# Performance work log

Measured on AMD Instinct MI355X. Metric: run time of the kernel, lower is better.

## Reference

```python
import jax, jax.numpy as jnp
import numpy as np

MEAN = 0.0
SIGMA = 2.0


def setup_inputs() -> dict:
    key = jax.random.key(0)
    B, S, D = 8, 1024, 1024
    ks = jax.random.split(key, 7)
    scale = 1.0 / np.sqrt(D)
    return {
        "x": jax.random.normal(ks[0], (B, S, D), dtype=jnp.float32),
        "Wa": jax.random.normal(ks[1], (D, D), dtype=jnp.float32) * scale,
        "ba": jnp.zeros((D,), dtype=jnp.float32),
        "Wshift": jax.random.normal(ks[2], (D, D), dtype=jnp.float32) * scale,
        "bshift": jnp.zeros((D,), dtype=jnp.float32),
        "Wscale": jax.random.normal(ks[3], (D, D), dtype=jnp.float32) * scale,
        "bscale": jnp.zeros((D,), dtype=jnp.float32),
    }


def _gaussian_matrix(S, dtype):
    # Row t holds the flipped, normalized Gaussian kernel of length t+1:
    # weight on position j (j<=t) is exp(-((t-j)-mean)^2/(2*sigma^2)), row-normalized.
    idx = jnp.arange(S)
    d = idx[:, None] - idx[None, :]  # t - j
    g = jnp.exp(-((d.astype(dtype) - MEAN) ** 2) / (2.0 * SIGMA ** 2))
    g = jnp.where(d >= 0, g, 0.0)  # causal (growing window)
    return g / jnp.sum(g, axis=1, keepdims=True)


def reference(x, Wa, ba, Wshift, bshift, Wscale, bscale):
    S = x.shape[1]
    W = _gaussian_matrix(S, x.dtype)  # [S, S] lower-triangular
    filtered = jnp.einsum("tj,bjd->btd", W, x)  # causal Gaussian-weighted sum
    shift = filtered @ Wshift + bshift
    scale = filtered @ Wscale + bscale
    affine = jax.nn.relu(x @ Wa + ba)
    return scale * affine + shift
```

## Files before the change

kernel.cpp:

```cpp
#include <hip/hip_runtime.h>
#include <stdint.h>

typedef __attribute__((ext_vector_type(8))) __bf16 bf16x8;
typedef __attribute__((ext_vector_type(4))) float f32x4;

__device__ __forceinline__ unsigned short f2bf(float f) {
  union { float f; unsigned int u; } v; v.f = f;
  unsigned int u = v.u;
  u = (u + 0x7FFFu + ((u >> 16) & 1u)) >> 16;
  return (unsigned short)u;
}
__device__ __forceinline__ float bf2f(unsigned int u) {
  union { unsigned int u; float f; } v; v.u = u << 16;
  return v.f;
}

__global__ __launch_bounds__(256) void prep(
    const float* __restrict__ x, unsigned short* __restrict__ xb,
    const float* __restrict__ Wa, const float* __restrict__ Wsh,
    const float* __restrict__ Wsc, unsigned short* __restrict__ Wt3)
{
  __shared__ float t[64][65];
  int bid = blockIdx.x;
  if (bid < 4096) {
    const size_t i = ((size_t)bid * 256 + threadIdx.x) * 8;
    const float4 a = *(const float4*)(x + i);
    const float4 b = *(const float4*)(x + i + 4);
    ushort4 o0, o1;
    o0.x = f2bf(a.x); o0.y = f2bf(a.y); o0.z = f2bf(a.z); o0.w = f2bf(a.w);
    o1.x = f2bf(b.x); o1.y = f2bf(b.y); o1.z = f2bf(b.z); o1.w = f2bf(b.w);
    *(ushort4*)(xb + i) = o0;
    *(ushort4*)(xb + i + 4) = o1;
    return;
  }
  bid -= 4096;
  const int z  = bid >> 8;
  const int yy = (bid >> 4) & 15;
  const int xx = bid & 15;
  const float* W = (z == 0) ? Wa : (z == 1) ? Wsh : Wsc;
  unsigned short* O = Wt3 + ((size_t)z << 20);
  const int k0 = xx * 64;
  const int n0 = yy * 64;
  const int r = threadIdx.x >> 4;
  const int c4 = threadIdx.x & 15;
#pragma unroll
  for (int i = 0; i < 4; ++i) {
    const int row = r + i * 16;
    const float4 v = *(const float4*)(W + (size_t)(k0 + row) * 1024 + n0 + c4 * 4);
    t[row][c4 * 4 + 0] = v.x; t[row][c4 * 4 + 1] = v.y;
    t[row][c4 * 4 + 2] = v.z; t[row][c4 * 4 + 3] = v.w;
  }
  __syncthreads();
#pragma unroll
  for (int i = 0; i < 4; ++i) {
    const int nr = r + i * 16;
    ushort4 o;
    o.x = f2bf(t[c4 * 4 + 0][nr]);
    o.y = f2bf(t[c4 * 4 + 1][nr]);
    o.z = f2bf(t[c4 * 4 + 2][nr]);
    o.w = f2bf(t[c4 * 4 + 3][nr]);
    *(ushort4*)(O + (size_t)(n0 + nr) * 1024 + k0 + c4 * 4) = o;
  }
}

__global__ __launch_bounds__(512, 2) void gemm_all(
    const unsigned short* __restrict__ xb, const unsigned short* __restrict__ Wt3,
    const float* __restrict__ ba, const float* __restrict__ bsh,
    const float* __restrict__ bsc, float* __restrict__ out)
{
  __shared__ __attribute__((aligned(16))) char lds[118784];
  unsigned short* const sX0 = (unsigned short*)lds;
  unsigned short* const sX1 = (unsigned short*)(lds + 34816);
  unsigned short* const sB0 = (unsigned short*)(lds + 69632);
  unsigned short* const sB1 = (unsigned short*)(lds + 94208);
  unsigned short* const ysh_l = (unsigned short*)lds;
  unsigned short* const ysc_l = (unsigned short*)(lds + 35072);
  unsigned short* const aff_l = (unsigned short*)(lds + 70144);

  const int tid = threadIdx.x;
  const int lane = tid & 63;
  const int wid = tid >> 6;
  const int wm = wid >> 1;
  const int wn = wid & 1;
  const int lr = lane & 15;
  const int lk = lane >> 4;

  const int bid = blockIdx.x;
  const int xcd = bid & 7;
  const int rr_ = bid >> 3;
  const int ntl = rr_ & 15;
  const int mg  = rr_ >> 4;
  const int bm0 = (xcd + (mg << 3)) * 256;
  const int bn0 = ntl * 64;
  const bool first = ((bm0 & 1023) == 0);

  f32x4 acc[3][4][2];
  f32x4 hacc[2][2];
  const f32x4 z = {0.f, 0.f, 0.f, 0.f};
#pragma unroll
  for (int a = 0; a < 3; ++a)
#pragma unroll
    for (int m = 0; m < 4; ++m)
#pragma unroll
      for (int j = 0; j < 2; ++j) acc[a][m][j] = z;
#pragma unroll
  for (int a = 0; a < 2; ++a)
#pragma unroll
    for (int j = 0; j < 2; ++j) hacc[a][j] = z;

  auto stage = [&](int k0, unsigned short* dX, unsigned short* dB) {
#pragma unroll
    for (int p = 0; p < 4; ++p) {
      const int po = (p * 512 + tid) * 16;
      const int row = po >> 7;
      const int lo = po ^ ((row & 7) << 4);
      const int colu = (lo & 127) >> 1;
      const unsigned short* src = xb + (size_t)(bm0 + row) * 1024 + k0 + colu;
      __builtin_amdgcn_global_load_lds(
          (const __attribute__((address_space(1))) void*)src,
          (__attribute__((address_space(3))) void*)(dX + (p * 512 + (wid << 6)) * 8),
          16, 0, 0);
    }
    if (tid < 128) {
      const int po = (2048 + tid) * 16;
      const int row = po >> 7;
      const int lo = po ^ ((row & 7) << 4);
      const int colu = (lo & 127) >> 1;
      int grow = bm0 - 16 + (row - 256);
      if (first) grow = bm0;
      const unsigned short* src = xb + (size_t)grow * 1024 + k0 + colu;
      __builtin_amdgcn_global_load_lds(
          (const __attribute__((address_space(1))) void*)src,
          (__attribute__((address_space(3))) void*)(dX + (2048 + (wid << 6)) * 8),
          16, 0, 0);
    }
#pragma unroll
    for (int mat = 0; mat < 3; ++mat) {
      const int po = tid * 16;
      const int row = po >> 7;
      const int lo = po ^ ((row & 7) << 4);
      const int colu = (lo & 127) >> 1;
      const unsigned short* src =
          Wt3 + ((size_t)mat << 20) + (size_t)(bn0 + row) * 1024 + k0 + colu;
      __builtin_amdgcn_global_load_lds(
          (const __attribute__((address_space(1))) void*)src,
          (__attribute__((address_space(3))) void*)(dB + mat * 4096 + (wid << 6) * 8),
          16, 0, 0);
    }
  };
  auto rd = [&](const unsigned short* base, int row, int s) -> bf16x8 {
    const int po = row * 128 + (((s * 32 + lk * 8) * 2) ^ ((row & 7) << 4));
    return *(const bf16x8*)((const char*)base + po);
  };

  stage(0, sX0, sB0);
  unsigned short *sXc = sX0, *sBc = sB0, *sXn = sX1, *sBn = sB1;

  for (int kt = 0; kt < 16; ++kt) {
    if (kt + 1 < 16) stage((kt + 1) * 64, sXn, sBn);

    if (kt + 1 < 16) {
      if (wid < 2) asm volatile("s_waitcnt vmcnt(8)" ::: "memory");
      else         asm volatile("s_waitcnt vmcnt(7)" ::: "memory");
    } else {
      asm volatile("s_waitcnt vmcnt(0)" ::: "memory");
    }
    __builtin_amdgcn_s_barrier();
    asm volatile("" ::: "memory");

#pragma unroll
    for (int s = 0; s < 2; ++s) {
      bf16x8 ax[4], bb[3][2], hax;
#pragma unroll
      for (int m = 0; m < 4; ++m)
        ax[m] = rd(sXc, wm * 64 + m * 16 + lr, s);
#pragma unroll
      for (int mat = 0; mat < 3; ++mat)
#pragma unroll
        for (int jj = 0; jj < 2; ++jj)
          bb[mat][jj] = rd(sBc + mat * 4096, wn * 32 + jj * 16 + lr, s);
      if (wm == 0) hax = rd(sXc, 256 + lr, s);

      __builtin_amdgcn_s_setprio(1);
#pragma unroll
      for (int m = 0; m < 4; ++m)
#pragma unroll
        for (int mat = 0; mat < 3; ++mat)
#pragma unroll
          for (int jj = 0; jj < 2; ++jj)
            acc[mat][m][jj] = __builtin_amdgcn_mfma_f32_16x16x32_bf16(
                ax[m], bb[mat][jj], acc[mat][m][jj], 0, 0, 0);
      if (wm == 0) {
#pragma unroll
        for (int mat = 1; mat < 3; ++mat)
#pragma unroll
          for (int jj = 0; jj < 2; ++jj)
            hacc[mat - 1][jj] = __builtin_amdgcn_mfma_f32_16x16x32_bf16(
                hax, bb[mat][jj], hacc[mat - 1][jj], 0, 0, 0);
      }
      __builtin_amdgcn_s_setprio(0);
    }

    asm volatile("s_waitcnt lgkmcnt(0)" ::: "memory");
    __builtin_amdgcn_s_barrier();
    asm volatile("" ::: "memory");

    unsigned short* t1 = sXc; sXc = sXn; sXn = t1;
    unsigned short* t2 = sBc; sBc = sBn; sBn = t2;
  }

#pragma unroll
  for (int jj = 0; jj < 2; ++jj) {
    const int nn = wn * 32 + jj * 16 + lr;
    const float Ba = ba[bn0 + nn];
#pragma unroll
    for (int m = 0; m < 4; ++m)
#pragma unroll
      for (int q = 0; q < 4; ++q) {
        const int rowL = wm * 64 + m * 16 + lk * 4 + q;
        aff_l[nn * 258 + rowL] = f2bf(fmaxf(acc[0][m][jj][q] + Ba, 0.0f));
        ysh_l[nn * 274 + 15 + rowL] = f2bf(acc[1][m][jj][q]);
        ysc_l[nn * 274 + 15 + rowL] = f2bf(acc[2][m][jj][q]);
      }
    if (wm == 0) {
#pragma unroll
      for (int q = 0; q < 4; ++q) {
        const int hr = lk * 4 + q;
        if (hr > 0) {
          ysh_l[nn * 274 + hr - 1] = f2bf(hacc[0][jj][q]);
          ysc_l[nn * 274 + hr - 1] = f2bf(hacc[1][jj][q]);
        }
      }
    }
  }
  __syncthreads();
  if (first) {
    for (int i = tid; i < 64 * 15; i += 512) {
      const int nn = i / 15, rw = i % 15;
      ysh_l[nn * 274 + rw] = 0;
      ysc_l[nn * 274 + rw] = 0;
    }
  }
  __syncthreads();

  {
    const int nn = tid & 63;
    const int t0 = (tid >> 6) * 32;
    float g[16];
#pragma unroll
    for (int k = 0; k < 16; ++k) g[k] = __expf(-(float)(k * k) * 0.125f);
    float nfull = 0.f;
#pragma unroll
    for (int k = 0; k < 16; ++k) nfull += g[k];
    const float invf = 1.0f / nfull;
    const float bs = bsh[bn0 + nn];
    const float bc = bsc[bn0 + nn];

    float psh[15], psc[15];
#pragma unroll
    for (int i = 0; i < 15; ++i) {
      psh[i] = bf2f(ysh_l[nn * 274 + t0 + i]);
      psc[i] = bf2f(ysc_l[nn * 274 + t0 + i]);
    }

    for (int c = 0; c < 2; ++c) {
      const int T = t0 + c * 16;
      float csh[16], csc[16], av[16];
#pragma unroll
      for (int u = 0; u < 16; ++u) {
        csh[u] = bf2f(ysh_l[nn * 274 + 15 + T + u]);
        csc[u] = bf2f(ysc_l[nn * 274 + 15 + T + u]);
        av[u]  = bf2f(aff_l[nn * 258 + T + u]);
      }
#pragma unroll
      for (int u = 0; u < 16; ++u) {
        float fs = 0.f, fc = 0.f;
#pragma unroll
        for (int k = 0; k < 16; ++k) {
          const int d = u - k;
          const float vs = (d >= 0) ? csh[d] : psh[15 + d];
          const float vc = (d >= 0) ? csc[d] : psc[15 + d];
          fs = fmaf(g[k], vs, fs);
          fc = fmaf(g[k], vc, fc);
        }
        float inv = invf;
        if (first && (T + u) < 15) {
          float sum = 0.f;
#pragma unroll
          for (int k = 0; k < 16; ++k) sum += (k <= T + u) ? g[k] : 0.f;
          inv = 1.0f / sum;
        }
        out[(size_t)(bm0 + T + u) * 1024 + bn0 + nn] =
            (fc * inv + bc) * av[u] + (fs * inv + bs);
      }
#pragma unroll
      for (int i = 0; i < 15; ++i) { psh[i] = csh[i + 1]; psc[i] = csc[i + 1]; }
    }
  }
}

extern "C" void kernel_launch(void* const* d_in, const int* in_sizes, int n_in,
                              void* d_out, int out_size, void* d_ws, size_t ws_size,
                              hipStream_t stream) {
  const float* x   = (const float*)d_in[0];
  const float* Wa  = (const float*)d_in[1];
  const float* ba  = (const float*)d_in[2];
  const float* Wsh = (const float*)d_in[3];
  const float* bsh = (const float*)d_in[4];
  const float* Wsc = (const float*)d_in[5];
  const float* bsc = (const float*)d_in[6];
  float* out = (float*)d_out;

  char* ws = (char*)d_ws;
  unsigned short* xb  = (unsigned short*)(ws);
  unsigned short* Wt3 = (unsigned short*)(ws + (16u << 20));

  hipLaunchKernelGGL(prep, dim3(4096 + 768), dim3(256), 0, stream,
                     x, xb, Wa, Wsh, Wsc, Wt3);
  hipLaunchKernelGGL(gemm_all, dim3(512), dim3(512), 0, stream,
                     xb, Wt3, ba, bsh, bsc, out);
}
```

Measured before the change: 79.39 us.

## Switch GEMM mainloop to triple-buffered K=32 stages with precomputed load addresses

The fused three-matrix GEMM loop moves from double-buffered K=64 tiles to a three-slot ring of K=32 tiles, prefetching two stages ahead. Global-to-LDS source addresses and destination offsets are computed once per thread, and the copy work is spread across all waves with a new two-rows-per-128B-line swizzle. The aim is to keep more memory traffic in flight, hide load latency, and shrink the LDS footprint. The cost is twice as many barriers per K step and hand-tuned vmcnt counts that must match the per-wave load counts exactly.

```diff
diff --git a/kernel.cpp b/kernel.cpp
--- a/kernel.cpp
+++ b/kernel.cpp
@@ -68,11 +68,8 @@
     const float* __restrict__ ba, const float* __restrict__ bsh,
     const float* __restrict__ bsc, float* __restrict__ out)
 {
-  __shared__ __attribute__((aligned(16))) char lds[118784];
-  unsigned short* const sX0 = (unsigned short*)lds;
-  unsigned short* const sX1 = (unsigned short*)(lds + 34816);
-  unsigned short* const sB0 = (unsigned short*)(lds + 69632);
-  unsigned short* const sB1 = (unsigned short*)(lds + 94208);
+  __shared__ __attribute__((aligned(16))) char lds[103168];
+  constexpr int SLOT = 29696;
   unsigned short* const ysh_l = (unsigned short*)lds;
   unsigned short* const ysc_l = (unsigned short*)(lds + 35072);
   unsigned short* const aff_l = (unsigned short*)(lds + 70144);
@@ -108,105 +105,104 @@
 #pragma unroll
     for (int j = 0; j < 2; ++j) hacc[a][j] = z;
 
-  auto stage = [&](int k0, unsigned short* dX, unsigned short* dB) {
+  const unsigned short* sbase[4];
+  int doff[4];
+#pragma unroll
+  for (int p = 0; p < 4; ++p) {
+    const int gid = p * 8 + wid;
+    sbase[p] = nullptr; doff[p] = 0;
+    if (gid < 17) {
+      const int po = gid * 1024 + (lane << 4);
+      const int line = po >> 7;
+      const int il = (po & 127) ^ ((line & 7) << 4);
+      const int row = line * 2 + (il >> 6);
+      const int colu = (il & 63) >> 1;
+      int grow = (row < 256) ? (bm0 + row)
+                             : (first ? bm0 : bm0 - 16 + (row - 256));
+      sbase[p] = xb + (size_t)grow * 1024 + colu;
+      doff[p] = gid * 1024;
+    } else if (gid < 29) {
+      const int pb = (gid - 17) * 1024 + (lane << 4);
+      const int line = pb >> 7;
+      const int il = (pb & 127) ^ ((line & 7) << 4);
+      const int mat = line >> 5;
+      const int rowm = ((line & 31) << 1) + (il >> 6);
+      const int colu = (il & 63) >> 1;
+      sbase[p] = Wt3 + ((size_t)mat << 20) + (size_t)(bn0 + rowm) * 1024 + colu;
+      doff[p] = 17408 + (gid - 17) * 1024;
+    }
+  }
+
+  auto stage = [&](int k0, char* slot) {
 #pragma unroll
     for (int p = 0; p < 4; ++p) {
-      const int po = (p * 512 + tid) * 16;
-      const int row = po >> 7;
-      const int lo = po ^ ((row & 7) << 4);
-      const int colu = (lo & 127) >> 1;
-      const unsigned short* src = xb + (size_t)(bm0 + row) * 1024 + k0 + colu;
-      __builtin_amdgcn_global_load_lds(
-          (const __attribute__((address_space(1))) void*)src,
-          (__attribute__((address_space(3))) void*)(dX + (p * 512 + (wid << 6)) * 8),
-          16, 0, 0);
-    }
-    if (tid < 128) {
-      const int po = (2048 + tid) * 16;
-      const int row = po >> 7;
-      const int lo = po ^ ((row & 7) << 4);
-      const int colu = (lo & 127) >> 1;
-      int grow = bm0 - 16 + (row - 256);
-      if (first) grow = bm0;
-      const unsigned short* src = xb + (size_t)grow * 1024 + k0 + colu;
-      __builtin_amdgcn_global_load_lds(
-          (const __attribute__((address_space(1))) void*)src,
-          (__attribute__((address_space(3))) void*)(dX + (2048 + (wid << 6)) * 8),
-          16, 0, 0);
-    }
-#pragma unroll
-    for (int mat = 0; mat < 3; ++mat) {
-      const int po = tid * 16;
-      const int row = po >> 7;
-      const int lo = po ^ ((row & 7) << 4);
-      const int colu = (lo & 127) >> 1;
-      const unsigned short* src =
-          Wt3 + ((size_t)mat << 20) + (size_t)(bn0 + row) * 1024 + k0 + colu;
-      __builtin_amdgcn_global_load_lds(
-          (const __attribute__((address_space(1))) void*)src,
-          (__attribute__((address_space(3))) void*)(dB + mat * 4096 + (wid << 6) * 8),
-          16, 0, 0);
+      if (p * 8 + wid < 29) {
+        __builtin_amdgcn_global_load_lds(
+            (const __attribute__((address_space(1))) void*)(sbase[p] + k0),
+            (__attribute__((address_space(3))) void*)(slot + doff[p]), 16, 0, 0);
+      }
     }
   };
-  auto rd = [&](const unsigned short* base, int row, int s) -> bf16x8 {
-    const int po = row * 128 + (((s * 32 + lk * 8) * 2) ^ ((row & 7) << 4));
-    return *(const bf16x8*)((const char*)base + po);
+  auto rd = [&](const char* base, int row) -> bf16x8 {
+    const int po = (row >> 1) * 128 +
+        ((((row & 1) << 6) | (lk << 4)) ^ (((row >> 1) & 7) << 4));
+    return *(const bf16x8*)(base + po);
   };
 
-  stage(0, sX0, sB0);
-  unsigned short *sXc = sX0, *sBc = sB0, *sXn = sX1, *sBn = sB1;
-
-  for (int kt = 0; kt < 16; ++kt) {
-    if (kt + 1 < 16) stage((kt + 1) * 64, sXn, sBn);
-
-    if (kt + 1 < 16) {
-      if (wid < 2) asm volatile("s_waitcnt vmcnt(8)" ::: "memory");
-      else         asm volatile("s_waitcnt vmcnt(7)" ::: "memory");
+  char *s0 = lds, *s1 = lds + SLOT, *s2 = lds + 2 * SLOT;
+  stage(0, s0);
+  stage(32, s1);
+
+  for (int kt = 0; kt < 32; ++kt) {
+    if (kt + 2 < 32) stage((kt + 2) * 32, s2);
+
+    if (kt < 30) {
+      if (wid < 5) asm volatile("s_waitcnt vmcnt(8)" ::: "memory");
+      else         asm volatile("s_waitcnt vmcnt(6)" ::: "memory");
+    } else if (kt == 30) {
+      if (wid < 5) asm volatile("s_waitcnt vmcnt(4)" ::: "memory");
+      else         asm volatile("s_waitcnt vmcnt(3)" ::: "memory");
     } else {
       asm volatile("s_waitcnt vmcnt(0)" ::: "memory");
     }
     __builtin_amdgcn_s_barrier();
     asm volatile("" ::: "memory");
 
-#pragma unroll
-    for (int s = 0; s < 2; ++s) {
-      bf16x8 ax[4], bb[3][2], hax;
-#pragma unroll
-      for (int m = 0; m < 4; ++m)
-        ax[m] = rd(sXc, wm * 64 + m * 16 + lr, s);
+    bf16x8 ax[4], bb[3][2], hax;
+#pragma unroll
+    for (int m = 0; m < 4; ++m)
+      ax[m] = rd(s0, wm * 64 + m * 16 + lr);
+#pragma unroll
+    for (int mat = 0; mat < 3; ++mat)
+#pragma unroll
+      for (int jj = 0; jj < 2; ++jj)
+        bb[mat][jj] = rd(s0 + 17408 + mat * 4096, wn * 32 + jj * 16 + lr);
+    if (wm == 0) hax = rd(s0, 256 + lr);
+
+    __builtin_amdgcn_s_setprio(1);
+#pragma unroll
+    for (int m = 0; m < 4; ++m)
 #pragma unroll
       for (int mat = 0; mat < 3; ++mat)
 #pragma unroll
         for (int jj = 0; jj < 2; ++jj)
-          bb[mat][jj] = rd(sBc + mat * 4096, wn * 32 + jj * 16 + lr, s);
-      if (wm == 0) hax = rd(sXc, 256 + lr, s);
-
-      __builtin_amdgcn_s_setprio(1);
-#pragma unroll
-      for (int m = 0; m < 4; ++m)
-#pragma unroll
-        for (int mat = 0; mat < 3; ++mat)
-#pragma unroll
-          for (int jj = 0; jj < 2; ++jj)
-            acc[mat][m][jj] = __builtin_amdgcn_mfma_f32_16x16x32_bf16(
-                ax[m], bb[mat][jj], acc[mat][m][jj], 0, 0, 0);
-      if (wm == 0) {
-#pragma unroll
-        for (int mat = 1; mat < 3; ++mat)
-#pragma unroll
-          for (int jj = 0; jj < 2; ++jj)
-            hacc[mat - 1][jj] = __builtin_amdgcn_mfma_f32_16x16x32_bf16(
-                hax, bb[mat][jj], hacc[mat - 1][jj], 0, 0, 0);
-      }
-      __builtin_amdgcn_s_setprio(0);
-    }
+          acc[mat][m][jj] = __builtin_amdgcn_mfma_f32_16x16x32_bf16(
+              ax[m], bb[mat][jj], acc[mat][m][jj], 0, 0, 0);
+    if (wm == 0) {
+#pragma unroll
+      for (int mat = 1; mat < 3; ++mat)
+#pragma unroll
+        for (int jj = 0; jj < 2; ++jj)
+          hacc[mat - 1][jj] = __builtin_amdgcn_mfma_f32_16x16x32_bf16(
+              hax, bb[mat][jj], hacc[mat - 1][jj], 0, 0, 0);
+    }
+    __builtin_amdgcn_s_setprio(0);
 
     asm volatile("s_waitcnt lgkmcnt(0)" ::: "memory");
     __builtin_amdgcn_s_barrier();
     asm volatile("" ::: "memory");
 
-    unsigned short* t1 = sXc; sXc = sXn; sXn = t1;
-    unsigned short* t2 = sBc; sBc = sBn; sBn = t2;
+    char* tmp = s0; s0 = s1; s1 = s2; s2 = tmp;
   }
 
 #pragma unroll
```

Measured after the change: 86.16 us. 8.5% more time.
